# Kernel tuning notes

Measured on AMD Instinct MI355X. Metric: run time of the kernel, lower is better.

Reference implementation:

```python
import jax, jax.numpy as jnp
import numpy as np
import math

EMBED = 768
HEADS = 12
DK = EMBED // HEADS
FFN = 3072
NQ = 8
B, S = 4, 2048


def _layernorm(x, g, b, eps=1e-5):
    mu = jnp.mean(x, axis=-1, keepdims=True)
    var = jnp.var(x, axis=-1, keepdims=True)
    return (x - mu) * jax.lax.rsqrt(var + eps) * g + b


def setup_inputs() -> dict:
    key = jax.random.key(0)
    ks = jax.random.split(key, 16)
    std = 0.02
    inp = {
        "x": jax.random.normal(ks[0], (B, S, EMBED), dtype=jnp.float32),
        "mask": jnp.ones((B, S), dtype=jnp.int32),
        # attention projections (torch Linear: W [out, in])
        "wq": jax.random.normal(ks[1], (EMBED, EMBED), jnp.float32) * std,
        "bq": jnp.zeros((EMBED,), jnp.float32),
        "wk": jax.random.normal(ks[2], (EMBED, EMBED), jnp.float32) * std,
        "bk": jnp.zeros((EMBED,), jnp.float32),
        "wv": jax.random.normal(ks[3], (EMBED, EMBED), jnp.float32) * std,
        "bv": jnp.zeros((EMBED,), jnp.float32),
        "wo": jax.random.normal(ks[4], (EMBED, EMBED), jnp.float32) * std,
        "bo": jnp.zeros((EMBED,), jnp.float32),
        # layernorms
        "g1": jnp.ones((EMBED,), jnp.float32),
        "be1": jnp.zeros((EMBED,), jnp.float32),
        "g2": jnp.ones((EMBED,), jnp.float32),
        "be2": jnp.zeros((EMBED,), jnp.float32),
        # quantum FFN: trainable RY angles + two linears
        "theta": jax.random.normal(ks[5], (NQ,), jnp.float32) * 0.1,
        "w1": jax.random.normal(ks[6], (FFN, NQ), jnp.float32) * std,
        "b1": jnp.zeros((FFN,), jnp.float32),
        "w2": jax.random.normal(ks[7], (EMBED, FFN), jnp.float32) * std,
        "b2": jnp.zeros((EMBED,), jnp.float32),
    }
    return inp


def _block(x, mask, wq, bq, wk, bk, wv, bv, wo, bo, g1, be1, g2, be2,
           theta, w1, b1, w2, b2):
    b, s, _ = x.shape
    # --- multi-head attention (dropout = identity at eval) ---
    q = (x @ wq.T + bq).reshape(b, s, HEADS, DK)
    k = (x @ wk.T + bk).reshape(b, s, HEADS, DK)
    v = (x @ wv.T + bv).reshape(b, s, HEADS, DK)
    scores = jnp.einsum("bqhd,bkhd->bhqk", q, k) / math.sqrt(DK)
    scores = jnp.where(mask[:, None, None, :] == 0, -1e9, scores)
    attn = jax.nn.softmax(scores, axis=-1)
    ctx = jnp.einsum("bhqk,bkhd->bqhd", attn, v).reshape(b, s, EMBED)
    attn_out = ctx @ wo.T + bo
    x = _layernorm(x + attn_out, g1, be1)
    # --- quantum FFN: RY(x_i) then RY(theta_i) on |0>, <Z> = cos(x_i+theta_i)
    # (product state, no entanglement -> exact closed form, fully batched)
    meas = jnp.cos(x[..., :NQ] + theta)            # [b, s, NQ]
    h = jax.nn.relu(meas @ w1.T + b1)              # [b, s, FFN]
    ffn_out = h @ w2.T + b2                        # [b, s, EMBED]
    return _layernorm(x + ffn_out, g2, be2)


def reference(x, mask, wq, bq, wk, bk, wv, bv, wo, bo, g1, be1, g2, be2,
              theta, w1, b1, w2, b2):
    return _block(x, mask, wq, bq, wk, bk, wv, bv, wo, bo,
                  g1, be1, g2, be2, theta, w1, b1, w2, b2)
```

## Files before the change

### kernel.cpp

```cpp
#include <hip/hip_runtime.h>
#include <hip/hip_bf16.h>


typedef __bf16 bf16_t;
typedef bf16_t bf16x4 __attribute__((ext_vector_type(4)));
typedef bf16_t bf16x8 __attribute__((ext_vector_type(8)));
typedef float floatx4 __attribute__((ext_vector_type(4)));

#define LOG2E 1.44269504088896f

__device__ __forceinline__ void gload16(const bf16_t* g, bf16_t* l) {
    __builtin_amdgcn_global_load_lds(
        (const __attribute__((address_space(1))) unsigned int*)g,
        (__attribute__((address_space(3))) unsigned int*)l,
        16, 0, 0);
}

__global__ __launch_bounds__(256)
void prep(const float* __restrict__ x,
          const float* __restrict__ wq, const float* __restrict__ wk,
          const float* __restrict__ wv, const float* __restrict__ wo,
          const float* __restrict__ w2, const float* __restrict__ w1,
          const float* __restrict__ bq, const float* __restrict__ bk,
          const float* __restrict__ bv,
          bf16_t* __restrict__ xb, bf16_t* __restrict__ wqkv,
          bf16_t* __restrict__ wob, bf16_t* __restrict__ w2b,
          bf16_t* __restrict__ w1b, float* __restrict__ bqkv)
{
    const int seg = blockIdx.y;
    const int idx = blockIdx.x * 256 + threadIdx.x;
    if (seg == 0) {
        if (idx >= 1572864) return;
        const float4 f = ((const float4*)x)[idx];
        bf16x4 o = {(bf16_t)f.x, (bf16_t)f.y, (bf16_t)f.z, (bf16_t)f.w};
        ((bf16x4*)xb)[idx] = o;
    } else if (seg == 1) {
        if (idx >= 442368) return;
        const int e = idx * 4;
        float4 f = (e < 589824) ? ((const float4*)wq)[idx]
                 : (e < 1179648) ? ((const float4*)wk)[idx - 147456]
                                 : ((const float4*)wv)[idx - 294912];
        if (e < 589824) { f.x *= 0.125f; f.y *= 0.125f; f.z *= 0.125f; f.w *= 0.125f; }
        bf16x4 o = {(bf16_t)f.x, (bf16_t)f.y, (bf16_t)f.z, (bf16_t)f.w};
        ((bf16x4*)wqkv)[idx] = o;
    } else if (seg == 2) {
        if (idx >= 147456) return;
        const float4 f = ((const float4*)wo)[idx];
        bf16x4 o = {(bf16_t)f.x, (bf16_t)f.y, (bf16_t)f.z, (bf16_t)f.w};
        ((bf16x4*)wob)[idx] = o;
    } else if (seg == 3) {
        if (idx >= 589824) return;
        const float4 f = ((const float4*)w2)[idx];
        bf16x4 o = {(bf16_t)f.x, (bf16_t)f.y, (bf16_t)f.z, (bf16_t)f.w};
        ((bf16x4*)w2b)[idx] = o;
    } else if (seg == 4) {
        if (idx >= 576) return;
        const int e = idx * 4;
        float4 f = (e < 768) ? ((const float4*)bq)[idx]
                 : (e < 1536) ? ((const float4*)bk)[idx - 192]
                              : ((const float4*)bv)[idx - 384];
        if (e < 768) { f.x *= 0.125f; f.y *= 0.125f; f.z *= 0.125f; f.w *= 0.125f; }
        ((float4*)bqkv)[idx] = f;
    } else {
        if (idx >= 6144) return;
        const float4 f = ((const float4*)w1)[idx];
        bf16x4 o = {(bf16_t)f.x, (bf16_t)f.y, (bf16_t)f.z, (bf16_t)f.w};
        ((bf16x4*)w1b)[idx] = o;
    }
}

template<typename TC>
__global__ __launch_bounds__(256)
void gemm_bb(const bf16_t* __restrict__ A, const bf16_t* __restrict__ W,
             const float* __restrict__ bias, TC* __restrict__ C,
             int kPer, int lda, int ldw, int ldc, int splitStride)
{
    __shared__ __align__(16) bf16_t As[2][4096];
    __shared__ __align__(16) bf16_t Bs[2][4096];
    const int tid  = threadIdx.x;
    const int wave = tid >> 6;
    const int lane = tid & 63;
    const int wm = (wave >> 1) * 64;
    const int wn = (wave & 1) * 64;

    const int nwg  = gridDim.x * gridDim.y;
    const int flat = blockIdx.y * gridDim.x + blockIdx.x;
    const int swzb = (flat & 7) * (nwg >> 3) + (flat >> 3);
    const int bm = (swzb / gridDim.x) * 128;
    const int bn = (swzb % gridDim.x) * 128;

    const int fr = lane & 15;
    const int fk = (lane >> 4) * 8;

    const int kBeg = blockIdx.z * kPer;
    const int kEnd = kBeg + kPer;
    C += (size_t)blockIdx.z * splitStride;

    const int srow = tid >> 2;
    const int scol = (tid & 3) * 8;

    floatx4 acc[4][4] = {};

    const bf16_t* gA = A + (size_t)(bm + srow) * lda + scol;
    const bf16_t* gB = W + (size_t)(bn + srow) * ldw + scol;

#define STAGE(buf, kk)                                              \
    {   const bf16_t* ga = gA + (kk);                               \
        const bf16_t* gb = gB + (kk);                               \
        gload16(ga,                    &As[buf][tid * 8]);          \
        gload16(ga + (size_t)64 * lda, &As[buf][tid * 8 + 2048]);   \
        gload16(gb,                    &Bs[buf][tid * 8]);          \
        gload16(gb + (size_t)64 * ldw, &Bs[buf][tid * 8 + 2048]);   \
    }

    STAGE(0, kBeg);
    __syncthreads();

    int cur = 0;
    for (int k0 = kBeg; k0 < kEnd; k0 += 32) {
        if (k0 + 32 < kEnd) STAGE(cur ^ 1, k0 + 32);

        bf16x8 fa[4], fb[4];
        #pragma unroll
        for (int i = 0; i < 4; ++i) {
            fa[i] = *(const bf16x8*)&As[cur][(wm + i * 16 + fr) * 32 + fk];
            fb[i] = *(const bf16x8*)&Bs[cur][(wn + i * 16 + fr) * 32 + fk];
        }
        #pragma unroll
        for (int mi = 0; mi < 4; ++mi)
            #pragma unroll
            for (int ni = 0; ni < 4; ++ni)
                acc[mi][ni] = __builtin_amdgcn_mfma_f32_16x16x32_bf16(
                    fa[mi], fb[ni], acc[mi][ni], 0, 0, 0);

        __syncthreads();
        cur ^= 1;
    }
#undef STAGE

    const int fg = (lane >> 4) * 4;
    const bool addb = (blockIdx.z == 0);
    #pragma unroll
    for (int mi = 0; mi < 4; ++mi) {
        #pragma unroll
        for (int ni = 0; ni < 4; ++ni) {
            const int col = bn + wn + ni * 16 + fr;
            const float bv = addb ? bias[col] : 0.f;
            #pragma unroll
            for (int r = 0; r < 4; ++r) {
                const int row = bm + wm + mi * 16 + fg + r;
                C[(size_t)row * ldc + col] = (TC)(acc[mi][ni][r] + bv);
            }
        }
    }
}

__global__ __launch_bounds__(256)
void gemm_qkv(const bf16_t* __restrict__ A, const bf16_t* __restrict__ W0,
              const float* __restrict__ bias0,
              bf16_t* __restrict__ Qb, bf16_t* __restrict__ Kh,
              bf16_t* __restrict__ Vh)
{
    __shared__ __align__(16) bf16_t As[2][4096];
    __shared__ __align__(16) bf16_t Bs[2][4096];
    const int tid  = threadIdx.x;
    const int wave = tid >> 6;
    const int lane = tid & 63;
    const int wm = (wave >> 1) * 64;
    const int wn = (wave & 1) * 64;

    const int nwg  = gridDim.x * gridDim.y;
    const int flat = blockIdx.y * gridDim.x + blockIdx.x;
    const int swzb = (flat & 7) * (nwg >> 3) + (flat >> 3);
    const int tx = swzb % gridDim.x;
    const int bm = (swzb / gridDim.x) * 128;
    const int sect = tx / 6;
    const int bn = (tx % 6) * 128;
    const bf16_t* W    = W0 + (size_t)sect * 589824;
    const float* bias  = bias0 + sect * 768;

    const int fr = lane & 15;
    const int fk = (lane >> 4) * 8;
    const int srow = tid >> 2;
    const int scol = (tid & 3) * 8;

    floatx4 acc[4][4] = {};

    const bf16_t* gA = A + (size_t)(bm + srow) * 768 + scol;
    const bf16_t* gB = W + (size_t)(bn + srow) * 768 + scol;

#define STAGEQ(buf, kk)                                             \
    {   const bf16_t* ga = gA + (kk);                               \
        const bf16_t* gb = gB + (kk);                               \
        gload16(ga,                   &As[buf][tid * 8]);           \
        gload16(ga + (size_t)64*768,  &As[buf][tid * 8 + 2048]);    \
        gload16(gb,                   &Bs[buf][tid * 8]);           \
        gload16(gb + (size_t)64*768,  &Bs[buf][tid * 8 + 2048]);    \
    }

    STAGEQ(0, 0);
    __syncthreads();

    int cur = 0;
    for (int k0 = 0; k0 < 768; k0 += 32) {
        if (k0 + 32 < 768) STAGEQ(cur ^ 1, k0 + 32);

        bf16x8 fa[4], fb[4];
        #pragma unroll
        for (int i = 0; i < 4; ++i) {
            fa[i] = *(const bf16x8*)&As[cur][(wm + i * 16 + fr) * 32 + fk];
            fb[i] = *(const bf16x8*)&Bs[cur][(wn + i * 16 + fr) * 32 + fk];
        }
        #pragma unroll
        for (int mi = 0; mi < 4; ++mi)
            #pragma unroll
            for (int ni = 0; ni < 4; ++ni)
                acc[mi][ni] = __builtin_amdgcn_mfma_f32_16x16x32_bf16(
                    fa[mi], fb[ni], acc[mi][ni], 0, 0, 0);

        __syncthreads();
        cur ^= 1;
    }
#undef STAGEQ

    const int fg = (lane >> 4) * 4;
    #pragma unroll
    for (int mi = 0; mi < 4; ++mi) {
        #pragma unroll
        for (int ni = 0; ni < 4; ++ni) {
            const int col = bn + wn + ni * 16 + fr;
            const float bv = bias[col];
            #pragma unroll
            for (int r = 0; r < 4; ++r) {
                const int row = bm + wm + mi * 16 + fg + r;
                const bf16_t val = (bf16_t)(acc[mi][ni][r] + bv);
                if (sect == 0) {
                    Qb[(size_t)row * 768 + col] = val;
                } else {
                    const int head = col >> 6;
                    const int d    = col & 63;
                    const size_t base =
                        ((size_t)((row >> 11) * 12 + head) * 2048 + (row & 2047)) * 64;
                    if (sect == 1)
                        Kh[base + (d ^ ((row & 7) << 3))] = val;
                    else
                        Vh[base + d] = val;
                }
            }
        }
    }
}

__global__ __launch_bounds__(256)
void attn_mfma(const bf16_t* __restrict__ Qb, const bf16_t* __restrict__ Kh,
               const bf16_t* __restrict__ Vh, const int* __restrict__ mask,
               bf16_t* __restrict__ ctx)
{
    __shared__ __align__(16) bf16_t KsL[2][4096];
    __shared__ bf16_t Vt[80][72];
    __shared__ float  mb_s[64];
    __shared__ bf16_t Pl[4][32][72];

    const int flat = blockIdx.x;
    const int swzb = (flat & 7) * 96 + (flat >> 3);
    const int bh = swzb >> 4;
    const int b = bh / 12, h = bh % 12;
    const int tid  = threadIdx.x;
    const int wave = tid >> 6;
    const int lane = tid & 63;
    const int g    = lane >> 4;
    const int fr   = lane & 15;
    const int qbase = (swzb & 15) * 128 + wave * 32;

    for (int idx = tid; idx < 16 * 72; idx += 256) {
        const int rr = idx / 72, cc = idx % 72;
        Vt[64 + rr][cc] = (bf16_t)(rr == 0 ? 1.f : 0.f);
    }

    bf16x8 qf[2][2];
    #pragma unroll
    for (int qt = 0; qt < 2; ++qt)
        #pragma unroll
        for (int s = 0; s < 2; ++s) {
            const size_t tok = (size_t)(b * 2048 + qbase + qt * 16 + fr);
            qf[qt][s] = *(const bf16x8*)(Qb + tok * 768 + h * 64 + s * 32 + g * 8);
        }

    floatx4 o[2][4] = {};
    floatx4 oe[2] = {};

    const bf16_t* kbase = Kh + (size_t)bh * 131072;
    const bf16_t* vbase = Vh + (size_t)bh * 131072;
    const int c0 = tid, c1 = tid + 256;

    gload16(kbase + c0 * 8, &KsL[0][c0 * 8]);
    gload16(kbase + c0 * 8 + 2048, &KsL[0][c0 * 8 + 2048]);
    bf16x8 rv0 = *(const bf16x8*)(vbase + c0 * 8);
    bf16x8 rv1 = *(const bf16x8*)(vbase + c1 * 8);
    float  rmb = (mask[b * 2048 + (tid & 63)] == 0) ? -1e9f : 0.f;

    int cur = 0;
    for (int kt = 0; kt < 32; ++kt) {
        __syncthreads();
        #pragma unroll
        for (int j = 0; j < 8; ++j) {
            Vt[(c0 & 7) * 8 + j][c0 >> 3] = rv0[j];
            Vt[(c1 & 7) * 8 + j][c1 >> 3] = rv1[j];
        }
        if (tid < 64) mb_s[tid] = rmb;
        __syncthreads();

        if (kt + 1 < 32) {
            const bf16_t* knext = kbase + (kt + 1) * 4096;
            gload16(knext + c0 * 8, &KsL[cur ^ 1][c0 * 8]);
            gload16(knext + c0 * 8 + 2048, &KsL[cur ^ 1][c0 * 8 + 2048]);
            const bf16_t* vnext = vbase + (kt + 1) * 4096;
            rv0 = *(const bf16x8*)(vnext + c0 * 8);
            rv1 = *(const bf16x8*)(vnext + c1 * 8);
            rmb = (mask[b * 2048 + (kt + 1) * 64 + (tid & 63)] == 0) ? -1e9f : 0.f;
        }

        floatx4 st_[2][4] = {};
        #pragma unroll
        for (int s = 0; s < 2; ++s) {
            bf16x8 kf[4];
            #pragma unroll
            for (int ct = 0; ct < 4; ++ct) {
                const int krow = ct * 16 + fr;
                const int kcol = (s * 32 + g * 8) ^ ((krow & 7) << 3);
                kf[ct] = *(const bf16x8*)&KsL[cur][krow * 64 + kcol];
            }
            #pragma unroll
            for (int qt = 0; qt < 2; ++qt)
                #pragma unroll
                for (int ct = 0; ct < 4; ++ct)
                    st_[qt][ct] = __builtin_amdgcn_mfma_f32_16x16x32_bf16(
                        kf[ct], qf[qt][s], st_[qt][ct], 0, 0, 0);
        }

        #pragma unroll
        for (int qt = 0; qt < 2; ++qt) {
            #pragma unroll
            for (int ct = 0; ct < 4; ++ct) {
                const float4 mb4 = *(const float4*)&mb_s[ct * 16 + g * 4];
                const float mbr[4] = { mb4.x, mb4.y, mb4.z, mb4.w };
                bf16x4 pw;
                #pragma unroll
                for (int r = 0; r < 4; ++r)
                    pw[r] = (bf16_t)__builtin_amdgcn_exp2f(
                        fmaf(st_[qt][ct][r], LOG2E, mbr[r]));
                *(bf16x4*)&Pl[wave][qt * 16 + fr][ct * 16 + g * 4] = pw;
            }
        }

        #pragma unroll
        for (int st2 = 0; st2 < 2; ++st2) {
            bf16x8 pf[2];
            #pragma unroll
            for (int qt = 0; qt < 2; ++qt)
                pf[qt] = *(const bf16x8*)&Pl[wave][qt * 16 + fr][st2 * 32 + g * 8];
            #pragma unroll
            for (int dt = 0; dt < 4; ++dt) {
                const bf16x8 vf = *(const bf16x8*)&Vt[dt * 16 + fr][st2 * 32 + g * 8];
                #pragma unroll
                for (int qt = 0; qt < 2; ++qt)
                    o[qt][dt] = __builtin_amdgcn_mfma_f32_16x16x32_bf16(
                        pf[qt], vf, o[qt][dt], 0, 0, 0);
            }
            const bf16x8 vo = *(const bf16x8*)&Vt[64 + fr][st2 * 32 + g * 8];
            #pragma unroll
            for (int qt = 0; qt < 2; ++qt)
                oe[qt] = __builtin_amdgcn_mfma_f32_16x16x32_bf16(
                    pf[qt], vo, oe[qt], 0, 0, 0);
        }

        cur ^= 1;
    }

    #pragma unroll
    for (int qt = 0; qt < 2; ++qt) {
        float inv[4];
        #pragma unroll
        for (int r = 0; r < 4; ++r) {
            const float lv = __shfl(oe[qt][r], (lane & 48), 64);
            inv[r] = 1.f / lv;
        }
        #pragma unroll
        for (int dt = 0; dt < 4; ++dt)
            #pragma unroll
            for (int r = 0; r < 4; ++r) {
                const size_t row = (size_t)(b * 2048 + qbase + qt * 16 + g * 4 + r);
                ctx[row * 768 + h * 64 + dt * 16 + fr] = (bf16_t)(o[qt][dt][r] * inv[r]);
            }
    }
}

__global__ __launch_bounds__(256)
void ln_fuse(const float* __restrict__ xin, const float* __restrict__ proj,
             const float* __restrict__ proj2,
             const float* __restrict__ g, const float* __restrict__ be,
             float* __restrict__ out,
             const float* __restrict__ theta, float* __restrict__ meas)
{
    const int wave = threadIdx.x >> 6;
    const int lane = threadIdx.x & 63;
    const int row  = blockIdx.x * 4 + wave;
    const size_t base = (size_t)row * 768;

    float4 v[3];
    float s1 = 0.f, s2 = 0.f;
    #pragma unroll
    for (int i = 0; i < 3; ++i) {
        const int c4 = lane + i * 64;
        const float4 a  = ((const float4*)(xin  + base))[c4];
        const float4 p  = ((const float4*)(proj + base))[c4];
        const float4 p2 = ((const float4*)(proj2 + base))[c4];
        v[i].x = a.x + p.x + p2.x;
        v[i].y = a.y + p.y + p2.y;
        v[i].z = a.z + p.z + p2.z;
        v[i].w = a.w + p.w + p2.w;
        s1 += v[i].x + v[i].y + v[i].z + v[i].w;
        s2 += v[i].x*v[i].x + v[i].y*v[i].y + v[i].z*v[i].z + v[i].w*v[i].w;
    }
    #pragma unroll
    for (int mk = 32; mk >= 1; mk >>= 1) {
        s1 += __shfl_xor(s1, mk, 64);
        s2 += __shfl_xor(s2, mk, 64);
    }
    const float mu   = s1 * (1.f / 768.f);
    const float var  = s2 * (1.f / 768.f) - mu * mu;
    const float rinv = rsqrtf(var + 1e-5f);

    #pragma unroll
    for (int i = 0; i < 3; ++i) {
        const int c4 = lane + i * 64;
        const float4 gg = ((const float4*)g)[c4];
        const float4 bb = ((const float4*)be)[c4];
        float4 o;
        o.x = (v[i].x - mu) * rinv * gg.x + bb.x;
        o.y = (v[i].y - mu) * rinv * gg.y + bb.y;
        o.z = (v[i].z - mu) * rinv * gg.z + bb.z;
        o.w = (v[i].w - mu) * rinv * gg.w + bb.w;
        ((float4*)(out + base))[c4] = o;
        if (i == 0 && meas != nullptr && lane < 2) {
            meas[row * 8 + lane * 4 + 0] = cosf(o.x + theta[lane * 4 + 0]);
            meas[row * 8 + lane * 4 + 1] = cosf(o.y + theta[lane * 4 + 1]);
            meas[row * 8 + lane * 4 + 2] = cosf(o.z + theta[lane * 4 + 2]);
            meas[row * 8 + lane * 4 + 3] = cosf(o.w + theta[lane * 4 + 3]);
        }
    }
}

__global__ __launch_bounds__(256)
void ffn1(const float* __restrict__ meas, const bf16_t* __restrict__ w1b,
          const float* __restrict__ b1, bf16_t* __restrict__ h)
{
    const int row0 = blockIdx.x * 4;
    __shared__ float ms[4][8];
    if (threadIdx.x < 32)
        ms[threadIdx.x >> 3][threadIdx.x & 7] = meas[row0 * 8 + threadIdx.x];
    __syncthreads();
    #pragma unroll
    for (int i = 0; i < 12; ++i) {
        const int f = threadIdx.x + i * 256;
        const bf16x8 w = *(const bf16x8*)(w1b + f * 8);
        float wv[8];
        #pragma unroll
        for (int j = 0; j < 8; ++j) wv[j] = (float)w[j];
        const float bias = b1[f];
        #pragma unroll
        for (int r = 0; r < 4; ++r) {
            float v = bias;
            #pragma unroll
            for (int j = 0; j < 8; ++j) v += ms[r][j] * wv[j];
            h[(size_t)(row0 + r) * 3072 + f] = (bf16_t)fmaxf(v, 0.f);
        }
    }
}

extern "C" void kernel_launch(void* const* d_in, const int* in_sizes, int n_in,
                              void* d_out, int out_size, void* d_ws, size_t ws_size,
                              hipStream_t stream)
{
    const float* x     = (const float*)d_in[0];
    const int*   mask  = (const int*)d_in[1];
    const float* wq    = (const float*)d_in[2];
    const float* bq    = (const float*)d_in[3];
    const float* wk    = (const float*)d_in[4];
    const float* bk    = (const float*)d_in[5];
    const float* wv    = (const float*)d_in[6];
    const float* bv    = (const float*)d_in[7];
    const float* wo    = (const float*)d_in[8];
    const float* bo    = (const float*)d_in[9];
    const float* g1    = (const float*)d_in[10];
    const float* be1   = (const float*)d_in[11];
    const float* g2    = (const float*)d_in[12];
    const float* be2   = (const float*)d_in[13];
    const float* theta = (const float*)d_in[14];
    const float* w1    = (const float*)d_in[15];
    const float* b1    = (const float*)d_in[16];
    const float* w2    = (const float*)d_in[17];
    const float* b2    = (const float*)d_in[18];
    float* out = (float*)d_out;

    char* ws = (char*)d_ws;
    bf16_t* Qb     = (bf16_t*)(ws + 0);
    bf16_t* Kh     = (bf16_t*)(ws + 12582912);
    bf16_t* Vh     = (bf16_t*)(ws + 25165824);
    bf16_t* ctx    = (bf16_t*)(ws + 37748736);
    float*  attnp  = (float*)(ws + 50331648);
    float*  y      = (float*)(ws + 100663296);
    float*  meas   = (float*)(ws + 125829120);
    bf16_t* xb     = (bf16_t*)(ws + 126091264);
    bf16_t* wqkv   = (bf16_t*)(ws + 138674176);
    bf16_t* wob    = (bf16_t*)(ws + 142213120);
    bf16_t* w2b    = (bf16_t*)(ws + 143392768);
    float*  bqkv   = (float*)(ws + 148111360);
    bf16_t* w1b    = (bf16_t*)(ws + 148120576);
    float*  ffnp   = (float*)(ws + 0);
    bf16_t* h      = (bf16_t*)(ws + 50331648);

    const dim3 blk(256);

    prep<<<dim3(6144, 6), blk, 0, stream>>>(x, wq, wk, wv, wo, w2, w1, bq, bk, bv,
                                            xb, wqkv, wob, w2b, w1b, bqkv);

    gemm_qkv<<<dim3(18, 64), blk, 0, stream>>>(xb, wqkv, bqkv, Qb, Kh, Vh);

    attn_mfma<<<dim3(768), blk, 0, stream>>>(Qb, Kh, Vh, mask, ctx);

    gemm_bb<float><<<dim3(6, 64, 2), blk, 0, stream>>>(
        ctx, wob, bo, attnp, 384, 768, 768, 768, 6291456);

    ln_fuse<<<dim3(2048), blk, 0, stream>>>(x, attnp, attnp + 6291456,
                                            g1, be1, y, theta, meas);

    ffn1<<<dim3(2048), blk, 0, stream>>>(meas, w1b, b1, h);

    gemm_bb<float><<<dim3(6, 64, 2), blk, 0, stream>>>(
        h, w2b, b2, ffnp, 1536, 3072, 3072, 768, 6291456);

    ln_fuse<<<dim3(2048), blk, 0, stream>>>(y, ffnp, ffnp + 6291456,
                                            g2, be2, out, nullptr, nullptr);
}
```

Baseline: 305.3 us.

## Store V pre-transposed and swizzled, async-load V tiles, precompute mask bias

The QKV GEMM epilogue now writes V transposed per head (d-major, with an XOR swizzle on the token index) using 4-wide stores. The attention kernel can then stream V tiles straight into LDS with global_load_lds, double-buffered like K, rather than loading into registers and transposing by hand through LDS. This removes a per-iteration LDS scatter and one of the two barriers. The mask is turned into a float bias once in the prep kernel and read from global memory inside the loop. In exchange, the epilogue stores for V become strided, and each iteration makes uncached global reads of the mask bias.

```diff
diff --git a/kernel.cpp b/kernel.cpp
--- a/kernel.cpp
+++ b/kernel.cpp
@@ -22,10 +22,11 @@
           const float* __restrict__ wv, const float* __restrict__ wo,
           const float* __restrict__ w2, const float* __restrict__ w1,
           const float* __restrict__ bq, const float* __restrict__ bk,
-          const float* __restrict__ bv,
+          const float* __restrict__ bv, const int* __restrict__ mask,
           bf16_t* __restrict__ xb, bf16_t* __restrict__ wqkv,
           bf16_t* __restrict__ wob, bf16_t* __restrict__ w2b,
-          bf16_t* __restrict__ w1b, float* __restrict__ bqkv)
+          bf16_t* __restrict__ w1b, float* __restrict__ bqkv,
+          float* __restrict__ mbf)
 {
     const int seg = blockIdx.y;
     const int idx = blockIdx.x * 256 + threadIdx.x;
@@ -61,11 +62,20 @@
                               : ((const float4*)bv)[idx - 384];
         if (e < 768) { f.x *= 0.125f; f.y *= 0.125f; f.z *= 0.125f; f.w *= 0.125f; }
         ((float4*)bqkv)[idx] = f;
-    } else {
+    } else if (seg == 5) {
         if (idx >= 6144) return;
         const float4 f = ((const float4*)w1)[idx];
         bf16x4 o = {(bf16_t)f.x, (bf16_t)f.y, (bf16_t)f.z, (bf16_t)f.w};
         ((bf16x4*)w1b)[idx] = o;
+    } else {
+        if (idx >= 2048) return;
+        const int4 m = ((const int4*)mask)[idx];
+        float4 f;
+        f.x = (m.x == 0) ? -1e9f : 0.f;
+        f.y = (m.y == 0) ? -1e9f : 0.f;
+        f.z = (m.z == 0) ? -1e9f : 0.f;
+        f.w = (m.w == 0) ? -1e9f : 0.f;
+        ((float4*)mbf)[idx] = f;
     }
 }
 
@@ -159,7 +169,7 @@
 void gemm_qkv(const bf16_t* __restrict__ A, const bf16_t* __restrict__ W0,
               const float* __restrict__ bias0,
               bf16_t* __restrict__ Qb, bf16_t* __restrict__ Kh,
-              bf16_t* __restrict__ Vh)
+              bf16_t* __restrict__ VhT)
 {
     __shared__ __align__(16) bf16_t As[2][4096];
     __shared__ __align__(16) bf16_t Bs[2][4096];
@@ -226,26 +236,39 @@
     const int fg = (lane >> 4) * 4;
     #pragma unroll
     for (int mi = 0; mi < 4; ++mi) {
+        const int row0 = bm + wm + mi * 16 + fg;
         #pragma unroll
         for (int ni = 0; ni < 4; ++ni) {
             const int col = bn + wn + ni * 16 + fr;
             const float bv = bias[col];
-            #pragma unroll
-            for (int r = 0; r < 4; ++r) {
-                const int row = bm + wm + mi * 16 + fg + r;
-                const bf16_t val = (bf16_t)(acc[mi][ni][r] + bv);
-                if (sect == 0) {
-                    Qb[(size_t)row * 768 + col] = val;
-                } else {
-                    const int head = col >> 6;
-                    const int d    = col & 63;
+            if (sect == 0) {
+                #pragma unroll
+                for (int r = 0; r < 4; ++r)
+                    Qb[(size_t)(row0 + r) * 768 + col] =
+                        (bf16_t)(acc[mi][ni][r] + bv);
+            } else if (sect == 1) {
+                const int head = col >> 6;
+                const int d    = col & 63;
+                #pragma unroll
+                for (int r = 0; r < 4; ++r) {
+                    const int row = row0 + r;
                     const size_t base =
                         ((size_t)((row >> 11) * 12 + head) * 2048 + (row & 2047)) * 64;
-                    if (sect == 1)
-                        Kh[base + (d ^ ((row & 7) << 3))] = val;
-                    else
-                        Vh[base + d] = val;
+                    Kh[base + (d ^ ((row & 7) << 3))] =
+                        (bf16_t)(acc[mi][ni][r] + bv);
                 }
+            } else {
+                const int head = col >> 6;
+                const int d    = col & 63;
+                bf16x4 v4;
+                #pragma unroll
+                for (int r = 0; r < 4; ++r)
+                    v4[r] = (bf16_t)(acc[mi][ni][r] + bv);
+                const int bhh = (row0 >> 11) * 12 + head;
+                const int t   = row0 & 2047;
+                const size_t idx = ((size_t)bhh * 64 + d) * 2048 +
+                                   (t & ~63) + ((t & 63) ^ ((d & 7) << 3));
+                *(bf16x4*)&VhT[idx] = v4;
             }
         }
     }
@@ -253,12 +276,12 @@
 
 __global__ __launch_bounds__(256)
 void attn_mfma(const bf16_t* __restrict__ Qb, const bf16_t* __restrict__ Kh,
-               const bf16_t* __restrict__ Vh, const int* __restrict__ mask,
+               const bf16_t* __restrict__ VhT, const float* __restrict__ mbf,
                bf16_t* __restrict__ ctx)
 {
-    __shared__ __align__(16) bf16_t KsL[2][4096];
-    __shared__ bf16_t Vt[80][72];
-    __shared__ float  mb_s[64];
+    __shared__ __align__(16) bf16_t Ks[2][4096];
+    __shared__ __align__(16) bf16_t Vt[2][4096];
+    __shared__ bf16_t Vones[16 * 72];
     __shared__ bf16_t Pl[4][32][72];
 
     const int flat = blockIdx.x;
@@ -272,10 +295,8 @@
     const int fr   = lane & 15;
     const int qbase = (swzb & 15) * 128 + wave * 32;
 
-    for (int idx = tid; idx < 16 * 72; idx += 256) {
-        const int rr = idx / 72, cc = idx % 72;
-        Vt[64 + rr][cc] = (bf16_t)(rr == 0 ? 1.f : 0.f);
-    }
+    for (int idx = tid; idx < 16 * 72; idx += 256)
+        Vones[idx] = (bf16_t)((idx < 72) ? 1.f : 0.f);
 
     bf16x8 qf[2][2];
     #pragma unroll
@@ -289,35 +310,27 @@
     floatx4 o[2][4] = {};
     floatx4 oe[2] = {};
 
-    const bf16_t* kbase = Kh + (size_t)bh * 131072;
-    const bf16_t* vbase = Vh + (size_t)bh * 131072;
-    const int c0 = tid, c1 = tid + 256;
-
-    gload16(kbase + c0 * 8, &KsL[0][c0 * 8]);
-    gload16(kbase + c0 * 8 + 2048, &KsL[0][c0 * 8 + 2048]);
-    bf16x8 rv0 = *(const bf16x8*)(vbase + c0 * 8);
-    bf16x8 rv1 = *(const bf16x8*)(vbase + c1 * 8);
-    float  rmb = (mask[b * 2048 + (tid & 63)] == 0) ? -1e9f : 0.f;
+    const bf16_t* kbase = Kh  + (size_t)bh * 131072;
+    const bf16_t* vbase = VhT + (size_t)bh * 131072;
+    const float*  mrow  = mbf + b * 2048;
+    const size_t  voff  = (size_t)(tid >> 3) * 2048 + (tid & 7) * 8;
+
+    gload16(kbase + tid * 8,        &Ks[0][tid * 8]);
+    gload16(kbase + tid * 8 + 2048, &Ks[0][tid * 8 + 2048]);
+    gload16(vbase + voff,             &Vt[0][tid * 8]);
+    gload16(vbase + voff + 32 * 2048, &Vt[0][tid * 8 + 2048]);
 
     int cur = 0;
     for (int kt = 0; kt < 32; ++kt) {
         __syncthreads();
-        #pragma unroll
-        for (int j = 0; j < 8; ++j) {
-            Vt[(c0 & 7) * 8 + j][c0 >> 3] = rv0[j];
-            Vt[(c1 & 7) * 8 + j][c1 >> 3] = rv1[j];
-        }
-        if (tid < 64) mb_s[tid] = rmb;
-        __syncthreads();
 
         if (kt + 1 < 32) {
-            const bf16_t* knext = kbase + (kt + 1) * 4096;
-            gload16(knext + c0 * 8, &KsL[cur ^ 1][c0 * 8]);
-            gload16(knext + c0 * 8 + 2048, &KsL[cur ^ 1][c0 * 8 + 2048]);
-            const bf16_t* vnext = vbase + (kt + 1) * 4096;
-            rv0 = *(const bf16x8*)(vnext + c0 * 8);
-            rv1 = *(const bf16x8*)(vnext + c1 * 8);
-            rmb = (mask[b * 2048 + (kt + 1) * 64 + (tid & 63)] == 0) ? -1e9f : 0.f;
+            const bf16_t* kn = kbase + (kt + 1) * 4096;
+            gload16(kn + tid * 8,        &Ks[cur ^ 1][tid * 8]);
+            gload16(kn + tid * 8 + 2048, &Ks[cur ^ 1][tid * 8 + 2048]);
+            const bf16_t* vn = vbase + (kt + 1) * 64;
+            gload16(vn + voff,             &Vt[cur ^ 1][tid * 8]);
+            gload16(vn + voff + 32 * 2048, &Vt[cur ^ 1][tid * 8 + 2048]);
         }
 
         floatx4 st_[2][4] = {};
@@ -328,7 +341,7 @@
             for (int ct = 0; ct < 4; ++ct) {
                 const int krow = ct * 16 + fr;
                 const int kcol = (s * 32 + g * 8) ^ ((krow & 7) << 3);
-                kf[ct] = *(const bf16x8*)&KsL[cur][krow * 64 + kcol];
+                kf[ct] = *(const bf16x8*)&Ks[cur][krow * 64 + kcol];
             }
             #pragma unroll
             for (int qt = 0; qt < 2; ++qt)
@@ -342,7 +355,7 @@
         for (int qt = 0; qt < 2; ++qt) {
             #pragma unroll
             for (int ct = 0; ct < 4; ++ct) {
-                const float4 mb4 = *(const float4*)&mb_s[ct * 16 + g * 4];
+                const float4 mb4 = *(const float4*)&mrow[kt * 64 + ct * 16 + g * 4];
                 const float mbr[4] = { mb4.x, mb4.y, mb4.z, mb4.w };
                 bf16x4 pw;
                 #pragma unroll
@@ -361,13 +374,15 @@
                 pf[qt] = *(const bf16x8*)&Pl[wave][qt * 16 + fr][st2 * 32 + g * 8];
             #pragma unroll
             for (int dt = 0; dt < 4; ++dt) {
-                const bf16x8 vf = *(const bf16x8*)&Vt[dt * 16 + fr][st2 * 32 + g * 8];
+                const int vrow = dt * 16 + fr;
+                const int vcol = (st2 * 32 + g * 8) ^ ((vrow & 7) << 3);
+                const bf16x8 vf = *(const bf16x8*)&Vt[cur][vrow * 64 + vcol];
                 #pragma unroll
                 for (int qt = 0; qt < 2; ++qt)
                     o[qt][dt] = __builtin_amdgcn_mfma_f32_16x16x32_bf16(
                         pf[qt], vf, o[qt][dt], 0, 0, 0);
             }
-            const bf16x8 vo = *(const bf16x8*)&Vt[64 + fr][st2 * 32 + g * 8];
+            const bf16x8 vo = *(const bf16x8*)&Vones[fr * 72 + st2 * 32 + g * 8];
             #pragma unroll
             for (int qt = 0; qt < 2; ++qt)
                 oe[qt] = __builtin_amdgcn_mfma_f32_16x16x32_bf16(
@@ -506,7 +521,7 @@
     char* ws = (char*)d_ws;
     bf16_t* Qb     = (bf16_t*)(ws + 0);
     bf16_t* Kh     = (bf16_t*)(ws + 12582912);
-    bf16_t* Vh     = (bf16_t*)(ws + 25165824);
+    bf16_t* VhT    = (bf16_t*)(ws + 25165824);
     bf16_t* ctx    = (bf16_t*)(ws + 37748736);
     float*  attnp  = (float*)(ws + 50331648);
     float*  y      = (float*)(ws + 100663296);
@@ -517,17 +532,18 @@
     bf16_t* w2b    = (bf16_t*)(ws + 143392768);
     float*  bqkv   = (float*)(ws + 148111360);
     bf16_t* w1b    = (bf16_t*)(ws + 148120576);
+    float*  mbf    = (float*)(ws + 148169728);
     float*  ffnp   = (float*)(ws + 0);
     bf16_t* h      = (bf16_t*)(ws + 50331648);
 
     const dim3 blk(256);
 
-    prep<<<dim3(6144, 6), blk, 0, stream>>>(x, wq, wk, wv, wo, w2, w1, bq, bk, bv,
-                                            xb, wqkv, wob, w2b, w1b, bqkv);
-
-    gemm_qkv<<<dim3(18, 64), blk, 0, stream>>>(xb, wqkv, bqkv, Qb, Kh, Vh);
-
-    attn_mfma<<<dim3(768), blk, 0, stream>>>(Qb, Kh, Vh, mask, ctx);
+    prep<<<dim3(6144, 7), blk, 0, stream>>>(x, wq, wk, wv, wo, w2, w1, bq, bk, bv,
+                                            mask, xb, wqkv, wob, w2b, w1b, bqkv, mbf);
+
+    gemm_qkv<<<dim3(18, 64), blk, 0, stream>>>(xb, wqkv, bqkv, Qb, Kh, VhT);
+
+    attn_mfma<<<dim3(768), blk, 0, stream>>>(Qb, Kh, VhT, mbf, ctx);
 
     gemm_bb<float><<<dim3(6, 64, 2), blk, 0, stream>>>(
         ctx, wob, bo, attnp, 384, 768, 768, 768, 6291456);
```

New measurement: 282.6 us. -7.5%, faster.
